# Kernel tuning notes

Measured on AMD Instinct MI355X. Metric: run time of the kernel, lower is better.

## Reference

```python
import math
import jax, jax.numpy as jnp
import numpy as np

B, S, D, N, H = 4, 1024, 1024, 16, 64

def setup_inputs() -> dict:
    key = jax.random.key(0)
    ks = jax.random.split(key, 10)
    sc = 0.02
    return {
        'from_tensor': jax.random.normal(ks[0], (B, S, D), jnp.float32),
        'to_tensor': jax.random.normal(ks[1], (B, S, D), jnp.float32),
        'attention_mask': jnp.ones((B, S, S), jnp.int32),
        'wq': jax.random.normal(ks[2], (D, N, H), jnp.float32) * sc,
        'bq': jnp.zeros((N, H), jnp.float32),
        'wk': jax.random.normal(ks[3], (D, N, H), jnp.float32) * sc,
        'bk': jnp.zeros((N, H), jnp.float32),
        'wv': jax.random.normal(ks[4], (D, N, H), jnp.float32) * sc,
        'bv': jnp.zeros((N, H), jnp.float32),
        'pre_softmax_weight': jax.random.normal(ks[5], (N, N), jnp.float32) * sc,
        'post_softmax_weight': jax.random.normal(ks[6], (N, N), jnp.float32) * sc,
        'wo': jax.random.normal(ks[7], (N, H, D), jnp.float32) * sc,
        'bo': jnp.zeros((D,), jnp.float32),
    }

def reference(from_tensor, to_tensor, attention_mask, wq, bq, wk, bk, wv, bv,
              pre_softmax_weight, post_softmax_weight, wo, bo):
    # QKV projections: [B,S,D] x [D,N,H] -> [B,S,N,H]
    q = jnp.einsum('bfd,dnh->bfnh', from_tensor, wq) + bq
    k = jnp.einsum('btd,dnh->btnh', to_tensor, wk) + bk
    v = jnp.einsum('btd,dnh->btnh', to_tensor, wv) + bv
    # attention scores [B,N,F,T]
    scores = jnp.einsum('btnh,bfnh->bnft', k, q) * (1.0 / math.sqrt(float(H)))
    # pre-softmax head mixing
    scores = jnp.einsum('bnft,nl->blft', scores, pre_softmax_weight)
    # masked softmax (mask expanded at axis 1, additive -10000 on masked)
    mask = attention_mask.astype(scores.dtype)[:, None, :, :]  # [B,1,F,T]
    scores = scores + (1.0 - mask) * -10000.0
    probs = jax.nn.softmax(scores, axis=-1)
    # post-softmax head mixing (dropout rate 0.0 -> identity)
    probs = jnp.einsum('bnft,nl->blft', probs, post_softmax_weight)
    # attend to values and project out
    ctx = jnp.einsum('bnft,btnh->bfnh', probs, v)
    out = jnp.einsum('bfnh,nhd->bfd', ctx, wo) + bo
    return out
```

## Files before the change

kernel.cpp:

```cpp
#include <hip/hip_runtime.h>
#include <hip/hip_bf16.h>

typedef __hip_bfloat16 bf16;
using short8 = __attribute__((ext_vector_type(8))) short;
using f32x4  = __attribute__((ext_vector_type(4))) float;
using f32x2  = __attribute__((ext_vector_type(2))) float;

#ifndef __has_builtin
#define __has_builtin(x) 0
#endif
#if __has_builtin(__builtin_amdgcn_global_load_lds)
#define HAVE_GLL 1
#else
#define HAVE_GLL 0
#endif

__device__ inline void stage16(const short* __restrict__ g, short* l, int lane) {
#if HAVE_GLL
  __builtin_amdgcn_global_load_lds((__attribute__((address_space(1))) void*)g,
                                   (__attribute__((address_space(3))) void*)l,
                                   16, 0, 0);
#else
  *(short8*)(l + lane * 8) = *(const short8*)g;
#endif
}

__device__ inline unsigned pack2bf(float a, float b) {
  bf16 h0 = __float2bfloat16(a), h1 = __float2bfloat16(b);
  return (unsigned)*(unsigned short*)&h0 | ((unsigned)*(unsigned short*)&h1 << 16);
}

__device__ inline f32x2 pk_fma(f32x2 a, f32x2 b, f32x2 c) {
#if defined(__gfx950__)
  f32x2 d;
  asm("v_pk_fma_f32 %0, %1, %2, %3" : "=v"(d) : "v"(a), "v"(b), "v"(c));
  return d;
#else
  return a * b + c;
#endif
}

__device__ inline f32x2 splat2(float s) { return (f32x2){s, s}; }

__global__ __launch_bounds__(256) void gemm_lds64(
    const bf16* __restrict__ Ag, long a_bs1, long a_bs2, int lda,
    const bf16* __restrict__ Bg, long b_bs1, long b_bs2, int ldb,
    void* __restrict__ Cg, long c_bs1, long c_bs2, int ldc,
    const float* __restrict__ bias, int K, int Z2, float alpha, int cf32)
{
  __shared__ short As[128 * 64];
  __shared__ short Bs[64 * 64];

  int z = blockIdx.z, z1 = z / Z2, z2 = z - z1 * Z2;
  const short* A = (const short*)(Ag + z1 * a_bs1 + z2 * a_bs2);
  const short* B = (const short*)(Bg + z1 * b_bs1 + z2 * b_bs2);

  int tid = threadIdx.x, lane = tid & 63, w = tid >> 6;
  int wm = w & 1, wn = w >> 1;
  int m0 = blockIdx.x * 128, n0 = blockIdx.y * 64;
  int r = lane & 15, q = lane >> 4;

  int srow = lane >> 3, scol = (lane & 7) * 8;
  const short* Asrc = A + (long)(m0 + w * 32 + srow) * lda + scol;
  const short* Bsrc = B + (long)(n0 + w * 16 + srow) * ldb + scol;
  short* Adst = As + (w * 32) * 64;
  short* Bdst = Bs + (w * 16) * 64;

  f32x4 acc[4][2];
  #pragma unroll
  for (int i = 0; i < 4; ++i)
    #pragma unroll
    for (int j = 0; j < 2; ++j) acc[i][j] = (f32x4){0.f, 0.f, 0.f, 0.f};

  for (int kt = 0; kt < K; kt += 64) {
    #pragma unroll
    for (int i = 0; i < 4; ++i)
      stage16(Asrc + (long)i * 8 * lda + kt, Adst + i * 8 * 64, lane);
    #pragma unroll
    for (int i = 0; i < 2; ++i)
      stage16(Bsrc + (long)i * 8 * ldb + kt, Bdst + i * 8 * 64, lane);
    __syncthreads();
    #pragma unroll
    for (int kk = 0; kk < 64; kk += 32) {
      short8 af[4], bfr[2];
      #pragma unroll
      for (int i = 0; i < 4; ++i)
        af[i] = *(const short8*)&As[(wm * 64 + i * 16 + r) * 64 + kk + q * 8];
      #pragma unroll
      for (int j = 0; j < 2; ++j)
        bfr[j] = *(const short8*)&Bs[(wn * 32 + j * 16 + r) * 64 + kk + q * 8];
      #pragma unroll
      for (int i = 0; i < 4; ++i)
        #pragma unroll
        for (int j = 0; j < 2; ++j)
          acc[i][j] = __builtin_amdgcn_mfma_f32_16x16x32_bf16(af[i], bfr[j], acc[i][j], 0, 0, 0);
    }
    __syncthreads();
  }

  long cb = z1 * c_bs1 + z2 * c_bs2;
  #pragma unroll
  for (int j = 0; j < 2; ++j) {
    int col = n0 + wn * 32 + j * 16 + r;
    float bv = bias ? bias[col] : 0.0f;
    #pragma unroll
    for (int i = 0; i < 4; ++i) {
      int row0 = m0 + wm * 64 + i * 16 + q * 4;
      #pragma unroll
      for (int rr = 0; rr < 4; ++rr) {
        float val = acc[i][j][rr] * alpha + bv;
        long idx = cb + (long)(row0 + rr) * ldc + col;
        if (cf32) ((float*)Cg)[idx] = val;
        else ((bf16*)Cg)[idx] = __float2bfloat16(val);
      }
    }
  }
}

struct QKVArgs {
  const bf16* A[3];
  const bf16* Bw[3];
  bf16* C[3];
  const float* bias[3];
};

__global__ __launch_bounds__(256) void gemm_qkv(QKVArgs args) {
  __shared__ short As[128 * 64];
  __shared__ short Bs[64 * 64];

  int z = blockIdx.z;
  const short* A = (const short*)args.A[z];
  const short* B = (const short*)args.Bw[z];
  bf16* C = args.C[z];
  const float* bias = args.bias[z];

  int tid = threadIdx.x, lane = tid & 63, w = tid >> 6;
  int wm = w & 1, wn = w >> 1;
  int m0 = blockIdx.x * 128, n0 = blockIdx.y * 64;
  int r = lane & 15, q = lane >> 4;

  int srow = lane >> 3, scol = (lane & 7) * 8;
  const short* Asrc = A + (long)(m0 + w * 32 + srow) * 1024 + scol;
  const short* Bsrc = B + (long)(n0 + w * 16 + srow) * 1024 + scol;
  short* Adst = As + (w * 32) * 64;
  short* Bdst = Bs + (w * 16) * 64;

  f32x4 acc[4][2];
  #pragma unroll
  for (int i = 0; i < 4; ++i)
    #pragma unroll
    for (int j = 0; j < 2; ++j) acc[i][j] = (f32x4){0.f, 0.f, 0.f, 0.f};

  for (int kt = 0; kt < 1024; kt += 64) {
    #pragma unroll
    for (int i = 0; i < 4; ++i)
      stage16(Asrc + (long)i * 8 * 1024 + kt, Adst + i * 8 * 64, lane);
    #pragma unroll
    for (int i = 0; i < 2; ++i)
      stage16(Bsrc + (long)i * 8 * 1024 + kt, Bdst + i * 8 * 64, lane);
    __syncthreads();
    #pragma unroll
    for (int kk = 0; kk < 64; kk += 32) {
      short8 af[4], bfr[2];
      #pragma unroll
      for (int i = 0; i < 4; ++i)
        af[i] = *(const short8*)&As[(wm * 64 + i * 16 + r) * 64 + kk + q * 8];
      #pragma unroll
      for (int j = 0; j < 2; ++j)
        bfr[j] = *(const short8*)&Bs[(wn * 32 + j * 16 + r) * 64 + kk + q * 8];
      #pragma unroll
      for (int i = 0; i < 4; ++i)
        #pragma unroll
        for (int j = 0; j < 2; ++j)
          acc[i][j] = __builtin_amdgcn_mfma_f32_16x16x32_bf16(af[i], bfr[j], acc[i][j], 0, 0, 0);
    }
    __syncthreads();
  }

  #pragma unroll
  for (int j = 0; j < 2; ++j) {
    int col = n0 + wn * 32 + j * 16 + r;
    float bv = bias[col];
    #pragma unroll
    for (int i = 0; i < 4; ++i) {
      int row0 = m0 + wm * 64 + i * 16 + q * 4;
      #pragma unroll
      for (int rr = 0; rr < 4; ++rr)
        C[(long)(row0 + rr) * 1024 + col] = __float2bfloat16(acc[i][j][rr] + bv);
    }
  }
}

__global__ __launch_bounds__(256) void gemm_k64(
    const bf16* __restrict__ Ag, long a_bs1, long a_bs2, int lda,
    const bf16* __restrict__ Bg, long b_bs1, long b_bs2, int ldb,
    bf16* __restrict__ Cg, long c_bs1, long c_bs2, int ldc,
    int Z2, float alpha)
{
  int z = blockIdx.z, z1 = z / Z2, z2 = z - z1 * Z2;
  const short* A = (const short*)(Ag + z1 * a_bs1 + z2 * a_bs2);
  const short* B = (const short*)(Bg + z1 * b_bs1 + z2 * b_bs2);
  bf16* C = Cg + z1 * c_bs1 + z2 * c_bs2;

  int tid = threadIdx.x, lane = tid & 63, w = tid >> 6;
  int wm = w & 1, wn = w >> 1;
  int m0 = blockIdx.x * 128 + wm * 64;
  int n0 = blockIdx.y * 128 + wn * 64;
  int r = lane & 15, q = lane >> 4;

  const short* Ar = A + (long)(m0 + r) * lda + q * 8;
  const short* Br = B + (long)(n0 + r) * ldb + q * 8;

  f32x4 acc[4][4];
  #pragma unroll
  for (int i = 0; i < 4; ++i)
    #pragma unroll
    for (int j = 0; j < 4; ++j) acc[i][j] = (f32x4){0.f, 0.f, 0.f, 0.f};

  #pragma unroll
  for (int kk = 0; kk < 64; kk += 32) {
    short8 af[4], bfr[4];
    #pragma unroll
    for (int i = 0; i < 4; ++i) af[i] = *(const short8*)(Ar + (long)i * 16 * lda + kk);
    #pragma unroll
    for (int j = 0; j < 4; ++j) bfr[j] = *(const short8*)(Br + (long)j * 16 * ldb + kk);
    #pragma unroll
    for (int i = 0; i < 4; ++i)
      #pragma unroll
      for (int j = 0; j < 4; ++j)
        acc[i][j] = __builtin_amdgcn_mfma_f32_16x16x32_bf16(af[i], bfr[j], acc[i][j], 0, 0, 0);
  }

  #pragma unroll
  for (int j = 0; j < 4; ++j) {
    int col = n0 + j * 16 + r;
    #pragma unroll
    for (int i = 0; i < 4; ++i) {
      int row0 = m0 + i * 16 + q * 4;
      #pragma unroll
      for (int rr = 0; rr < 4; ++rr)
        C[(long)(row0 + rr) * ldc + col] = __float2bfloat16(acc[i][j][rr] * alpha);
    }
  }
}

__global__ __launch_bounds__(256) void cvt2(
    const float* __restrict__ a, const float* __restrict__ b,
    bf16* __restrict__ oa, bf16* __restrict__ ob)
{
  const float* in = blockIdx.y ? b : a;
  bf16* out = blockIdx.y ? ob : oa;
  int i = (blockIdx.x * 256 + threadIdx.x) * 8;
  float4 v0 = *(const float4*)(in + i);
  float4 v1 = *(const float4*)(in + i + 4);
  uint4 pk;
  pk.x = pack2bf(v0.x, v0.y);
  pk.y = pack2bf(v0.z, v0.w);
  pk.z = pack2bf(v1.x, v1.y);
  pk.w = pack2bf(v1.z, v1.w);
  *(uint4*)(out + i) = pk;
}

struct WT4 { const float* s[4]; bf16* d[4]; };

__global__ __launch_bounds__(256) void wtrans4(WT4 a) {
  __shared__ bf16 tile[64][66];
  int z = blockIdx.z;
  const float* in = a.s[z];
  bf16* out = a.d[z];
  int r0 = blockIdx.x * 64, c0 = blockIdx.y * 64;
  int tx = threadIdx.x & 63, ty = threadIdx.x >> 6;
  #pragma unroll
  for (int i = 0; i < 16; ++i) {
    int rr = i * 4 + ty;
    tile[rr][tx] = __float2bfloat16(in[(long)(r0 + rr) * 1024 + c0 + tx]);
  }
  __syncthreads();
  #pragma unroll
  for (int i = 0; i < 16; ++i) {
    int rr = i * 4 + ty;
    out[(long)(c0 + rr) * 1024 + r0 + tx] = tile[tx][rr];
  }
}

__global__ __launch_bounds__(256) void transpose_bf16(
    const bf16* __restrict__ in, long i_bs1, long i_bs2, int i_rs,
    bf16* __restrict__ out, long o_bs1, long o_bs2, int o_rs, int Z2)
{
  __shared__ bf16 tile[64][66];
  int z = blockIdx.z, z1 = z / Z2, z2 = z - z1 * Z2;
  const bf16* ib = in + z1 * i_bs1 + z2 * i_bs2;
  bf16* ob = out + z1 * o_bs1 + z2 * o_bs2;
  int r0 = blockIdx.x * 64, c0 = blockIdx.y * 64;
  int tx = threadIdx.x & 63, ty = threadIdx.x >> 6;
  #pragma unroll
  for (int i = 0; i < 16; ++i) {
    int rr = i * 4 + ty;
    tile[rr][tx] = ib[(long)(r0 + rr) * i_rs + c0 + tx];
  }
  __syncthreads();
  #pragma unroll
  for (int i = 0; i < 16; ++i) {
    int rr = i * 4 + ty;
    ob[(long)(c0 + rr) * o_rs + r0 + tx] = tile[tx][rr];
  }
}

__global__ __launch_bounds__(512) void mixsoftmax5(
    bf16* __restrict__ sc, long sc_bs, const float* __restrict__ pre,
    const float* __restrict__ post, const int* __restrict__ mask)
{
  __shared__ float wpre[256], wpost[256];
  __shared__ f32x2 zbufp[8][512];
  __shared__ f32x2 zbuf2p[8][32];
  __shared__ f32x2 zinvp[8];
  int tid = threadIdx.x;
  int f = blockIdx.x, b = blockIdx.y;
  if (tid < 256) {
    wpre[tid] = pre[tid];
    wpost[tid] = post[tid];
  }
  __syncthreads();

  unsigned short* scb = (unsigned short*)(sc + (long)b * sc_bs) + ((long)f << 10);
  const int* mk = mask + ((long)b << 20) + ((long)f << 10);
  int tg = tid * 2;

  unsigned u[16];
  #pragma unroll
  for (int n = 0; n < 16; ++n)
    u[n] = *(const unsigned*)(scb + ((long)n << 20) + tg);
  int2 mm = *(const int2*)(mk + tg);
  float madd0 = (1.0f - (float)mm.x) * -10000.0f;
  float madd1 = (1.0f - (float)mm.y) * -10000.0f;

  f32x2 m0[8], m1[8];
  #pragma unroll
  for (int p = 0; p < 8; ++p) {
    m0[p] = splat2(madd0);
    m1[p] = splat2(madd1);
  }

  #pragma unroll
  for (int n = 0; n < 16; ++n) {
    unsigned lo = u[n];
    f32x2 sp0 = splat2(__uint_as_float((lo & 0xffffu) << 16));
    f32x2 sp1 = splat2(__uint_as_float(lo & 0xffff0000u));
    const float4* wr = (const float4*)&wpre[n * 16];
    #pragma unroll
    for (int g = 0; g < 4; ++g) {
      float4 wv = wr[g];
      f32x2 wa = {wv.x, wv.y}, wb = {wv.z, wv.w};
      m0[g * 2 + 0] = pk_fma(wa, sp0, m0[g * 2 + 0]);
      m0[g * 2 + 1] = pk_fma(wb, sp0, m0[g * 2 + 1]);
      m1[g * 2 + 0] = pk_fma(wa, sp1, m1[g * 2 + 0]);
      m1[g * 2 + 1] = pk_fma(wb, sp1, m1[g * 2 + 1]);
    }
  }

  #pragma unroll
  for (int p = 0; p < 8; ++p) {
    m0[p].x = __expf(m0[p].x);  m0[p].y = __expf(m0[p].y);
    m1[p].x = __expf(m1[p].x);  m1[p].y = __expf(m1[p].y);
    zbufp[p][tid] = m0[p] + m1[p];
  }
  __syncthreads();
  if (tid < 256) {
    int p = tid >> 5, c = tid & 31;
    const f32x2* zr = &zbufp[p][c * 16];
    f32x2 s = zr[0];
    #pragma unroll
    for (int i = 1; i < 16; ++i) s += zr[i];
    zbuf2p[p][c] = s;
  }
  __syncthreads();
  if (tid < 8) {
    f32x2 s = zbuf2p[tid][0];
    #pragma unroll
    for (int g = 1; g < 32; ++g) s += zbuf2p[tid][g];
    zinvp[tid] = (f32x2){1.0f / s.x, 1.0f / s.y};
  }
  __syncthreads();
  if (tid < 256) {
    int n = tid >> 4;
    float zi = (n & 1) ? zinvp[n >> 1].y : zinvp[n >> 1].x;
    wpost[tid] *= zi;
  }
  __syncthreads();

  f32x2 o0[8], o1[8];
  #pragma unroll
  for (int p = 0; p < 8; ++p) {
    o0[p] = splat2(0.0f);
    o1[p] = splat2(0.0f);
  }
  #pragma unroll
  for (int n = 0; n < 16; ++n) {
    int p = n >> 1;
    float e0 = (n & 1) ? m0[p].y : m0[p].x;
    float e1 = (n & 1) ? m1[p].y : m1[p].x;
    f32x2 sp0 = splat2(e0), sp1 = splat2(e1);
    const float4* wr = (const float4*)&wpost[n * 16];
    #pragma unroll
    for (int g = 0; g < 4; ++g) {
      float4 wv = wr[g];
      f32x2 wa = {wv.x, wv.y}, wb = {wv.z, wv.w};
      o0[g * 2 + 0] = pk_fma(wa, sp0, o0[g * 2 + 0]);
      o0[g * 2 + 1] = pk_fma(wb, sp0, o0[g * 2 + 1]);
      o1[g * 2 + 0] = pk_fma(wa, sp1, o1[g * 2 + 0]);
      o1[g * 2 + 1] = pk_fma(wb, sp1, o1[g * 2 + 1]);
    }
  }
  #pragma unroll
  for (int l = 0; l < 16; ++l) {
    int p = l >> 1;
    float a0 = (l & 1) ? o0[p].y : o0[p].x;
    float a1 = (l & 1) ? o1[p].y : o1[p].x;
    *(unsigned*)(scb + ((long)l << 20) + tg) = pack2bf(a0, a1);
  }
}

extern "C" void kernel_launch(void* const* d_in, const int* in_sizes, int n_in,
                              void* d_out, int out_size, void* d_ws, size_t ws_size,
                              hipStream_t stream) {
  const float* from = (const float*)d_in[0];
  const float* to   = (const float*)d_in[1];
  const int*  mask  = (const int*)d_in[2];
  const float* wq = (const float*)d_in[3];
  const float* bq = (const float*)d_in[4];
  const float* wk = (const float*)d_in[5];
  const float* bk = (const float*)d_in[6];
  const float* wv = (const float*)d_in[7];
  const float* bv = (const float*)d_in[8];
  const float* pre  = (const float*)d_in[9];
  const float* post = (const float*)d_in[10];
  const float* wo = (const float*)d_in[11];
  const float* bo = (const float*)d_in[12];
  float* out = (float*)d_out;

  bf16* W = (bf16*)d_ws;
  const long M1 = 1048576;
  bool big = ws_size >= (size_t)(85 * M1) * 2;

  bf16 *Sc, *fromB, *toB, *wqT, *wkT, *wvT, *woT, *Q, *Kp, *V, *Vt, *ctx;
  if (big) {
    Sc = W;                 fromB = W;            toB = W + 4 * M1;
    wqT = W + 8 * M1;       wkT = W + 9 * M1;     wvT = W + 10 * M1;
    woT = W + 64 * M1;      Q = W + 65 * M1;      Kp = W + 69 * M1;
    V = W + 73 * M1;        Vt = W + 77 * M1;     ctx = W + 81 * M1;
  } else {
    Sc = W;                 fromB = W;            toB = W + 4 * M1;
    wqT = W + 8 * M1;       wkT = W + 9 * M1;     wvT = W + 10 * M1;
    woT = W + 16 * M1;      Q = W + 17 * M1;      Kp = W + 21 * M1;
    V = W + 25 * M1;        Vt = W + 29 * M1;     ctx = W + 33 * M1;
  }

  dim3 blk(256);

  cvt2<<<dim3(2048, 2), blk, 0, stream>>>(from, to, fromB, toB);
  WT4 wt;
  wt.s[0] = wq; wt.s[1] = wk; wt.s[2] = wv; wt.s[3] = wo;
  wt.d[0] = wqT; wt.d[1] = wkT; wt.d[2] = wvT; wt.d[3] = woT;
  wtrans4<<<dim3(16, 16, 4), blk, 0, stream>>>(wt);

  QKVArgs qa;
  qa.A[0] = fromB; qa.A[1] = toB; qa.A[2] = toB;
  qa.Bw[0] = wqT;  qa.Bw[1] = wkT; qa.Bw[2] = wvT;
  qa.C[0] = Q;     qa.C[1] = Kp;  qa.C[2] = V;
  qa.bias[0] = bq; qa.bias[1] = bk; qa.bias[2] = bv;
  gemm_qkv<<<dim3(32, 16, 3), blk, 0, stream>>>(qa);

  transpose_bf16<<<dim3(16, 1, 64), blk, 0, stream>>>(V, M1, 64, 1024,
                                                      Vt, M1, 65536, 1024, 16);

  if (big) {
    gemm_k64<<<dim3(8, 8, 64), blk, 0, stream>>>(
        Q, M1, 64, 1024, Kp, M1, 64, 1024, Sc, 16 * M1, M1, 1024, 16, 0.125f);
    mixsoftmax5<<<dim3(1024, 4), dim3(512), 0, stream>>>(Sc, 16 * M1, pre, post, mask);
    gemm_lds64<<<dim3(8, 1, 64), blk, 0, stream>>>(
        Sc, 16 * M1, M1, 1024, Vt, M1, 65536, 1024, ctx, M1, 64, 1024, nullptr,
        1024, 16, 1.0f, 0);
  } else {
    for (int b = 0; b < 4; ++b) {
      gemm_k64<<<dim3(8, 8, 16), blk, 0, stream>>>(
          Q + b * M1, 0, 64, 1024, Kp + b * M1, 0, 64, 1024,
          Sc, 0, M1, 1024, 16, 0.125f);
      mixsoftmax5<<<dim3(1024, 1), dim3(512), 0, stream>>>(Sc, 0, pre, post, mask + b * M1);
      gemm_lds64<<<dim3(8, 1, 16), blk, 0, stream>>>(
          Sc, 0, M1, 1024, Vt + b * M1, 0, 65536, 1024,
          ctx + b * M1, 0, 64, 1024, nullptr, 1024, 16, 1.0f, 0);
    }
  }

  gemm_lds64<<<dim3(32, 16, 1), blk, 0, stream>>>(
      ctx, 0, 0, 1024, woT, 0, 0, 1024, out, 0, 0, 1024, bo, 1024, 1, 1.0f, 1);
}
```

Measured before the change: 345.8 us.

## Use MFMA for pre/post-softmax head mixing in the softmax kernel

Rewrites the mix-softmax kernel to stage the 16-head score column through LDS and compute the 16x16 head-mixing matrices with bf16 MFMA instructions instead of scalar packed FMAs. The mask add is folded into the MFMA accumulator input, exp values are written back to LDS, and the normalizer is reduced with shuffles and a small LDS buffer. It aims to cut VALU work, but the mixing weights and exp values are now rounded to bf16, and the output stores become 2-byte scattered writes rather than 4-byte ones.

```diff
diff --git a/kernel.cpp b/kernel.cpp
--- a/kernel.cpp
+++ b/kernel.cpp
@@ -29,18 +29,6 @@
   bf16 h0 = __float2bfloat16(a), h1 = __float2bfloat16(b);
   return (unsigned)*(unsigned short*)&h0 | ((unsigned)*(unsigned short*)&h1 << 16);
 }
-
-__device__ inline f32x2 pk_fma(f32x2 a, f32x2 b, f32x2 c) {
-#if defined(__gfx950__)
-  f32x2 d;
-  asm("v_pk_fma_f32 %0, %1, %2, %3" : "=v"(d) : "v"(a), "v"(b), "v"(c));
-  return d;
-#else
-  return a * b + c;
-#endif
-}
-
-__device__ inline f32x2 splat2(float s) { return (f32x2){s, s}; }
 
 __global__ __launch_bounds__(256) void gemm_lds64(
     const bf16* __restrict__ Ag, long a_bs1, long a_bs2, int lda,
@@ -306,117 +294,100 @@
   }
 }
 
-__global__ __launch_bounds__(512) void mixsoftmax5(
+__global__ __launch_bounds__(512) void mixsoftmax6(
     bf16* __restrict__ sc, long sc_bs, const float* __restrict__ pre,
     const float* __restrict__ post, const int* __restrict__ mask)
 {
-  __shared__ float wpre[256], wpost[256];
-  __shared__ f32x2 zbufp[8][512];
-  __shared__ f32x2 zbuf2p[8][32];
-  __shared__ f32x2 zinvp[8];
+  __shared__ short Sb[1024][24];
+  __shared__ float wpreS[256], wpostS[256];
+  __shared__ float zred[8][16];
+  __shared__ float zinvs[16];
+
   int tid = threadIdx.x;
+  int lane = tid & 63, w = tid >> 6;
+  int g = lane >> 4;
+  int l = lane & 15;
   int f = blockIdx.x, b = blockIdx.y;
-  if (tid < 256) {
-    wpre[tid] = pre[tid];
-    wpost[tid] = post[tid];
-  }
-  __syncthreads();
 
   unsigned short* scb = (unsigned short*)(sc + (long)b * sc_bs) + ((long)f << 10);
   const int* mk = mask + ((long)b << 20) + ((long)f << 10);
   int tg = tid * 2;
 
-  unsigned u[16];
-  #pragma unroll
-  for (int n = 0; n < 16; ++n)
-    u[n] = *(const unsigned*)(scb + ((long)n << 20) + tg);
-  int2 mm = *(const int2*)(mk + tg);
-  float madd0 = (1.0f - (float)mm.x) * -10000.0f;
-  float madd1 = (1.0f - (float)mm.y) * -10000.0f;
-
-  f32x2 m0[8], m1[8];
-  #pragma unroll
-  for (int p = 0; p < 8; ++p) {
-    m0[p] = splat2(madd0);
-    m1[p] = splat2(madd1);
+  if (tid < 256) {
+    wpreS[tid] = pre[tid];
+    wpostS[tid] = post[tid];
   }
 
   #pragma unroll
   for (int n = 0; n < 16; ++n) {
-    unsigned lo = u[n];
-    f32x2 sp0 = splat2(__uint_as_float((lo & 0xffffu) << 16));
-    f32x2 sp1 = splat2(__uint_as_float(lo & 0xffff0000u));
-    const float4* wr = (const float4*)&wpre[n * 16];
-    #pragma unroll
-    for (int g = 0; g < 4; ++g) {
-      float4 wv = wr[g];
-      f32x2 wa = {wv.x, wv.y}, wb = {wv.z, wv.w};
-      m0[g * 2 + 0] = pk_fma(wa, sp0, m0[g * 2 + 0]);
-      m0[g * 2 + 1] = pk_fma(wb, sp0, m0[g * 2 + 1]);
-      m1[g * 2 + 0] = pk_fma(wa, sp1, m1[g * 2 + 0]);
-      m1[g * 2 + 1] = pk_fma(wb, sp1, m1[g * 2 + 1]);
-    }
-  }
-
-  #pragma unroll
-  for (int p = 0; p < 8; ++p) {
-    m0[p].x = __expf(m0[p].x);  m0[p].y = __expf(m0[p].y);
-    m1[p].x = __expf(m1[p].x);  m1[p].y = __expf(m1[p].y);
-    zbufp[p][tid] = m0[p] + m1[p];
+    int nn = (n + (tid & 12)) & 15;
+    unsigned uu = *(const unsigned*)(scb + ((long)nn << 20) + tg);
+    Sb[tg][nn]     = (short)(uu & 0xffffu);
+    Sb[tg + 1][nn] = (short)(uu >> 16);
   }
   __syncthreads();
-  if (tid < 256) {
-    int p = tid >> 5, c = tid & 31;
-    const f32x2* zr = &zbufp[p][c * 16];
-    f32x2 s = zr[0];
-    #pragma unroll
-    for (int i = 1; i < 16; ++i) s += zr[i];
-    zbuf2p[p][c] = s;
-  }
+
+  short8 af1;
+  #pragma unroll
+  for (int i = 0; i < 8; ++i) {
+    int n = ((g & 1) << 3) + i;
+    bf16 hv = __float2bfloat16(wpreS[n * 16 + l]);
+    af1[i] = (g < 2) ? *(short*)&hv : (short)0;
+  }
+
+  f32x4 zacc = (f32x4){0.f, 0.f, 0.f, 0.f};
+  int tb = w * 128 + l;
+  #pragma unroll
+  for (int it = 0; it < 8; ++it) {
+    int t0 = tb + it * 16;
+    short8 bfr = *(const short8*)&Sb[t0][(g & 1) * 8];
+    float madd = (1.0f - (float)mk[t0]) * -10000.0f;
+    f32x4 cin = (f32x4){madd, madd, madd, madd};
+    f32x4 a = __builtin_amdgcn_mfma_f32_16x16x32_bf16(af1, bfr, cin, 0, 0, 0);
+    f32x4 e;
+    #pragma unroll
+    for (int j = 0; j < 4; ++j) e[j] = __expf(a[j]);
+    zacc += e;
+    uint2 pk;
+    pk.x = pack2bf(e[0], e[1]);
+    pk.y = pack2bf(e[2], e[3]);
+    *(uint2*)&Sb[t0][g * 4] = pk;
+  }
+
+  #pragma unroll
+  for (int m = 1; m < 16; m <<= 1) {
+    #pragma unroll
+    for (int j = 0; j < 4; ++j) zacc[j] += __shfl_xor(zacc[j], m, 64);
+  }
+  if (l == 0) *(f32x4*)&zred[w][g * 4] = zacc;
   __syncthreads();
-  if (tid < 8) {
-    f32x2 s = zbuf2p[tid][0];
-    #pragma unroll
-    for (int g = 1; g < 32; ++g) s += zbuf2p[tid][g];
-    zinvp[tid] = (f32x2){1.0f / s.x, 1.0f / s.y};
+  if (tid < 16) {
+    float z = 0.f;
+    #pragma unroll
+    for (int ww = 0; ww < 8; ++ww) z += zred[ww][tid];
+    zinvs[tid] = 1.0f / z;
   }
   __syncthreads();
-  if (tid < 256) {
-    int n = tid >> 4;
-    float zi = (n & 1) ? zinvp[n >> 1].y : zinvp[n >> 1].x;
-    wpost[tid] *= zi;
-  }
-  __syncthreads();
-
-  f32x2 o0[8], o1[8];
-  #pragma unroll
-  for (int p = 0; p < 8; ++p) {
-    o0[p] = splat2(0.0f);
-    o1[p] = splat2(0.0f);
-  }
-  #pragma unroll
-  for (int n = 0; n < 16; ++n) {
-    int p = n >> 1;
-    float e0 = (n & 1) ? m0[p].y : m0[p].x;
-    float e1 = (n & 1) ? m1[p].y : m1[p].x;
-    f32x2 sp0 = splat2(e0), sp1 = splat2(e1);
-    const float4* wr = (const float4*)&wpost[n * 16];
-    #pragma unroll
-    for (int g = 0; g < 4; ++g) {
-      float4 wv = wr[g];
-      f32x2 wa = {wv.x, wv.y}, wb = {wv.z, wv.w};
-      o0[g * 2 + 0] = pk_fma(wa, sp0, o0[g * 2 + 0]);
-      o0[g * 2 + 1] = pk_fma(wb, sp0, o0[g * 2 + 1]);
-      o1[g * 2 + 0] = pk_fma(wa, sp1, o1[g * 2 + 0]);
-      o1[g * 2 + 1] = pk_fma(wb, sp1, o1[g * 2 + 1]);
-    }
-  }
-  #pragma unroll
-  for (int l = 0; l < 16; ++l) {
-    int p = l >> 1;
-    float a0 = (l & 1) ? o0[p].y : o0[p].x;
-    float a1 = (l & 1) ? o1[p].y : o1[p].x;
-    *(unsigned*)(scb + ((long)l << 20) + tg) = pack2bf(a0, a1);
+
+  short8 af2;
+  #pragma unroll
+  for (int i = 0; i < 8; ++i) {
+    int n = ((g & 1) << 3) + i;
+    bf16 hv = __float2bfloat16(wpostS[n * 16 + l] * zinvs[n]);
+    af2[i] = (g < 2) ? *(short*)&hv : (short)0;
+  }
+
+  #pragma unroll
+  for (int it = 0; it < 8; ++it) {
+    int t0 = tb + it * 16;
+    short8 bE = *(const short8*)&Sb[t0][(g & 1) * 8];
+    f32x4 o = __builtin_amdgcn_mfma_f32_16x16x32_bf16(
+        af2, bE, (f32x4){0.f, 0.f, 0.f, 0.f}, 0, 0, 0);
+    #pragma unroll
+    for (int j = 0; j < 4; ++j) {
+      bf16 hv = __float2bfloat16(o[j]);
+      scb[((long)(g * 4 + j) << 20) + t0] = *(unsigned short*)&hv;
+    }
   }
 }
 
@@ -476,7 +447,7 @@
   if (big) {
     gemm_k64<<<dim3(8, 8, 64), blk, 0, stream>>>(
         Q, M1, 64, 1024, Kp, M1, 64, 1024, Sc, 16 * M1, M1, 1024, 16, 0.125f);
-    mixsoftmax5<<<dim3(1024, 4), dim3(512), 0, stream>>>(Sc, 16 * M1, pre, post, mask);
+    mixsoftmax6<<<dim3(1024, 4), dim3(512), 0, stream>>>(Sc, 16 * M1, pre, post, mask);
     gemm_lds64<<<dim3(8, 1, 64), blk, 0, stream>>>(
         Sc, 16 * M1, M1, 1024, Vt, M1, 65536, 1024, ctx, M1, 64, 1024, nullptr,
         1024, 16, 1.0f, 0);
@@ -485,7 +456,7 @@
       gemm_k64<<<dim3(8, 8, 16), blk, 0, stream>>>(
           Q + b * M1, 0, 64, 1024, Kp + b * M1, 0, 64, 1024,
           Sc, 0, M1, 1024, 16, 0.125f);
-      mixsoftmax5<<<dim3(1024, 1), dim3(512), 0, stream>>>(Sc, 0, pre, post, mask + b * M1);
+      mixsoftmax6<<<dim3(1024, 1), dim3(512), 0, stream>>>(Sc, 0, pre, post, mask + b * M1);
       gemm_lds64<<<dim3(8, 1, 16), blk, 0, stream>>>(
           Sc, 0, M1, 1024, Vt + b * M1, 0, 65536, 1024,
           ctx + b * M1, 0, 64, 1024, nullptr, 1024, 16, 1.0f, 0);
```

Result: no change. 343.3 us (-0.7%).
